# Kernel tuning notes

Measured on AMD Instinct MI355X. Metric: run time of the kernel, lower is better.

Reference implementation:

```python
import jax, jax.numpy as jnp
import numpy as np

N_SRC = 50000
N_DST = 50000
N_EDGES = 800000
D_IN = 256
NUM_HEADS = 8
OUT_DIM = 16
NEG_SLOPE = 0.2


def setup_inputs() -> dict:
    key = jax.random.key(0)
    ks = jax.random.split(key, 9)
    feat_src = jax.random.normal(ks[0], (N_SRC, D_IN), dtype=jnp.float32)
    feat_dst = jax.random.normal(ks[1], (N_DST, D_IN), dtype=jnp.float32)
    W_src = jax.random.normal(ks[2], (NUM_HEADS * OUT_DIM, D_IN), dtype=jnp.float32) * 0.05
    b_src = jax.random.normal(ks[3], (NUM_HEADS * OUT_DIM,), dtype=jnp.float32) * 0.05
    W_dst = jax.random.normal(ks[4], (NUM_HEADS * OUT_DIM, D_IN), dtype=jnp.float32) * 0.05
    b_dst = jax.random.normal(ks[5], (NUM_HEADS * OUT_DIM,), dtype=jnp.float32) * 0.05
    attn = jax.random.normal(ks[6], (NUM_HEADS, 2 * OUT_DIM), dtype=jnp.float32) * 0.1
    src_idx = jax.random.randint(ks[7], (N_EDGES,), 0, N_SRC, dtype=jnp.int32)
    dst_idx = jax.random.randint(ks[8], (N_EDGES,), 0, N_DST, dtype=jnp.int32)
    return {"feat_src": feat_src, "feat_dst": feat_dst, "W_src": W_src,
            "b_src": b_src, "W_dst": W_dst, "b_dst": b_dst, "attn": attn,
            "src_idx": src_idx, "dst_idx": dst_idx}


def reference(feat_src, feat_dst, W_src, b_src, W_dst, b_dst, attn, src_idx, dst_idx):
    # Node-type-specific linear transforms (feat_drop=0 at inference)
    hs = (feat_src @ W_src.T + b_src).reshape(N_SRC, NUM_HEADS, OUT_DIM)
    hd = (feat_dst @ W_dst.T + b_dst).reshape(N_DST, NUM_HEADS, OUT_DIM)
    # Per-node attention logits: el_i = <hs_i, a_l>, er_j = <hd_j, a_r>
    el = jnp.einsum('nkd,kd->nk', hs, attn[:, :OUT_DIM])  # (N_src, K)
    er = jnp.einsum('nkd,kd->nk', hd, attn[:, OUT_DIM:])  # (N_dst, K)
    # Edge scores: e_uv = LeakyReLU(el_u + er_v)
    e = el[src_idx] + er[dst_idx]                          # (E, K)
    e = jnp.where(e >= 0, e, NEG_SLOPE * e)
    # Edge softmax over incoming edges of each destination node
    m = jax.ops.segment_max(e, dst_idx, num_segments=N_DST)        # (N_dst, K)
    e_exp = jnp.exp(e - m[dst_idx])
    denom = jax.ops.segment_sum(e_exp, dst_idx, num_segments=N_DST)
    a = e_exp / denom[dst_idx]                             # (E, K)
    # Weighted neighbor aggregation: sum_u a_uv * hs_u
    msg = hs[src_idx] * a[:, :, None]                      # (E, K, d_out)
    out = jax.ops.segment_sum(msg, dst_idx, num_segments=N_DST)
    return out.reshape(N_DST, NUM_HEADS * OUT_DIM)
```

## Files before the change

### kernel.cpp

```cpp
#include <hip/hip_runtime.h>
#include <hip/hip_bf16.h>

#define N_SRCC 50000
#define N_DSTC 50000
#define N_EDG 800000
#define NBUK 500
#define DPB 100
#define BCAP 2048
#define EPB 3334
#define NPB 240
#define GEMB 391

typedef __attribute__((ext_vector_type(8))) short bf16x8;
typedef __attribute__((ext_vector_type(4))) float f32x4;
typedef __attribute__((ext_vector_type(8))) unsigned short us8;

__device__ inline short f2bf(float x) {
  __hip_bfloat16 b = __float2bfloat16(x);
  return *reinterpret_cast<short*>(&b);
}
__device__ inline float bf2f(unsigned hi16) {
  union { unsigned u; float f; } c; c.u = hi16 << 16; return c.f;
}

__global__ void fold_kernel(const float* __restrict__ Wsrc, const float* __restrict__ bsrc,
                            const float* __restrict__ Wdst, const float* __restrict__ bdst,
                            const float* __restrict__ attn,
                            float* __restrict__ U, float* __restrict__ Cc,
                            short* __restrict__ Wbf, short* __restrict__ Ubf,
                            int* __restrict__ bCur) {
  int t = blockIdx.x * blockDim.x + threadIdx.x;
  if (t < 4096) {
    int side = t >> 11;
    int r = (t >> 8) & 7;
    int c = t & 255;
    const float* W = side ? Wdst : Wsrc;
    float s = 0.f;
    #pragma unroll
    for (int d = 0; d < 16; d++)
      s += attn[r*32 + side*16 + d] * W[(r*16 + d)*256 + c];
    U[t] = s;
    if (side == 1) Ubf[r*256 + c] = f2bf(s);
    else           Ubf[2048 + t]  = 0;
    const float4* p = (const float4*)&Wsrc[t*8];
    float4 v0 = p[0], v1 = p[1];
    bf16x8 w;
    w[0]=f2bf(v0.x); w[1]=f2bf(v0.y); w[2]=f2bf(v0.z); w[3]=f2bf(v0.w);
    w[4]=f2bf(v1.x); w[5]=f2bf(v1.y); w[6]=f2bf(v1.z); w[7]=f2bf(v1.w);
    *(bf16x8*)&Wbf[t*8] = w;
  }
  if (t < 16) {
    int side = t >> 3, r = t & 7;
    const float* b = side ? bdst : bsrc;
    float s = 0.f;
    #pragma unroll
    for (int d = 0; d < 16; d++) s += attn[r*32 + side*16 + d] * b[r*16 + d];
    Cc[t] = s;
  }
  if (t < NBUK) bCur[t] = 0;
}

__global__ __launch_bounds__(256) void mega(
    const float* __restrict__ feat_src, const float* __restrict__ feat_dst,
    const short* __restrict__ Wbf, const short* __restrict__ Ubf,
    const float* __restrict__ bias, const float* __restrict__ attn,
    const float* __restrict__ Cc,
    const int* __restrict__ src, const int* __restrict__ dst,
    int* __restrict__ bCur, unsigned* __restrict__ bData,
    __hip_bfloat16* __restrict__ hsC, float* __restrict__ el,
    float* __restrict__ er) {
  __shared__ __align__(16) char smem[20480];
  int b = blockIdx.x;
  int t = threadIdx.x;

  if (b < NPB) {
    int* h   = (int*)smem;
    int* cur = (int*)(smem + 2048);
    for (int i = t; i < NBUK; i += 256) h[i] = 0;
    __syncthreads();
    int start = b * EPB;
    int end = min(start + EPB, N_EDG);
    for (int e = start + t; e < end; e += 256)
      atomicAdd(&h[dst[e] / DPB], 1);
    __syncthreads();
    for (int i = t; i < NBUK; i += 256) {
      int c = h[i];
      cur[i] = c ? atomicAdd(&bCur[i], c) : 0;
    }
    __syncthreads();
    for (int e = start + t; e < end; e += 256) {
      int d = dst[e], bk = d / DPB;
      int pos = atomicAdd(&cur[bk], 1);
      if (pos < BCAP)
        bData[(size_t)bk*BCAP + pos] = (unsigned)src[e] | ((unsigned)(d - bk*DPB) << 16);
    }
    return;
  }

  if (b < NPB + GEMB) {
    short (*As)[40] = (short(*)[40])smem;
    short (*Bs)[40] = (short(*)[40])(smem + 10240);
    int lane = t & 63, wid = t >> 6;
    int wr = wid >> 1, wc = wid & 1;
    int row0 = (b - NPB) * 128;
    int lr = lane & 15, lk = lane >> 4;
    int sr = t >> 1, skq = (t & 1) * 16;
    int gr = row0 + sr;
    f32x4 acc[4][4] = {};
    float4 pa0 = {}, pa1 = {}, pa2 = {}, pa3 = {};
    bf16x8 pb0, pb1;

    #define LOADA_HS(K0) { \
      if (gr < N_SRCC) { \
        const float4* p = (const float4*)&feat_src[(size_t)gr*256 + (K0) + skq]; \
        pa0 = p[0]; pa1 = p[1]; pa2 = p[2]; pa3 = p[3]; \
      } \
    }
    #define LOADB_HS(K0) { \
      pb0 = *(const bf16x8*)&Wbf[sr*256 + (K0) + skq]; \
      pb1 = *(const bf16x8*)&Wbf[sr*256 + (K0) + skq + 8]; \
    }

    LOADA_HS(0); LOADB_HS(0);
    for (int k0 = 0; k0 < 256; k0 += 32) {
      {
        bf16x8 t0, t1;
        t0[0]=f2bf(pa0.x); t0[1]=f2bf(pa0.y); t0[2]=f2bf(pa0.z); t0[3]=f2bf(pa0.w);
        t0[4]=f2bf(pa1.x); t0[5]=f2bf(pa1.y); t0[6]=f2bf(pa1.z); t0[7]=f2bf(pa1.w);
        t1[0]=f2bf(pa2.x); t1[1]=f2bf(pa2.y); t1[2]=f2bf(pa2.z); t1[3]=f2bf(pa2.w);
        t1[4]=f2bf(pa3.x); t1[5]=f2bf(pa3.y); t1[6]=f2bf(pa3.z); t1[7]=f2bf(pa3.w);
        *(bf16x8*)&As[sr][skq]     = t0;
        *(bf16x8*)&As[sr][skq + 8] = t1;
        *(bf16x8*)&Bs[sr][skq]     = pb0;
        *(bf16x8*)&Bs[sr][skq + 8] = pb1;
      }
      __syncthreads();
      if (k0 < 224) { LOADA_HS(k0 + 32); LOADB_HS(k0 + 32); }
      bf16x8 af[4], bfr[4];
      #pragma unroll
      for (int m = 0; m < 4; m++)
        af[m] = *(const bf16x8*)&As[wr*64 + m*16 + lr][lk*8];
      #pragma unroll
      for (int n = 0; n < 4; n++)
        bfr[n] = *(const bf16x8*)&Bs[wc*64 + n*16 + lr][lk*8];
      #pragma unroll
      for (int m = 0; m < 4; m++)
        #pragma unroll
        for (int n = 0; n < 4; n++)
          acc[m][n] = __builtin_amdgcn_mfma_f32_16x16x32_bf16(af[m], bfr[n], acc[m][n], 0, 0, 0);
      __syncthreads();
    }
    #undef LOADA_HS
    #undef LOADB_HS
    #pragma unroll
    for (int m = 0; m < 4; m++) {
      int r0 = row0 + wr*64 + m*16 + lk*4;
      #pragma unroll
      for (int n = 0; n < 4; n++) {
        int col = wc*64 + n*16 + lr;
        int h = wc*4 + n;
        float bv = bias[col];
        float al = attn[h*32 + lr];
        #pragma unroll
        for (int j = 0; j < 4; j++) {
          int gr2 = r0 + j;
          float hv = acc[m][n][j] + bv;
          if (gr2 < N_SRCC) hsC[(size_t)gr2*128 + col] = __float2bfloat16(hv);
          float p = hv * al;
          p += __shfl_xor(p, 1); p += __shfl_xor(p, 2);
          p += __shfl_xor(p, 4); p += __shfl_xor(p, 8);
          if (lr == 0 && gr2 < N_SRCC) el[gr2*8 + h] = p;
        }
      }
    }
    return;
  }

  {
    short (*As)[40]  = (short(*)[40])smem;
    short (*Bu)[264] = (short(*)[264])(smem + 10240);
    int lane = t & 63, wid = t >> 6;
    int row0 = (b - NPB - GEMB) * 128;
    int lr = lane & 15, lk = lane >> 4;
    int sr = t >> 1, skq = (t & 1) * 16;
    int gr = row0 + sr;
    #pragma unroll
    for (int i = 0; i < 2; i++) {
      int c = t + i*256;
      int r = c >> 5, ck = c & 31;
      *(bf16x8*)&Bu[r][ck*8] = *(const bf16x8*)&Ubf[r*256 + ck*8];
    }
    f32x4 acc[2] = {};
    float4 pa0 = {}, pa1 = {}, pa2 = {}, pa3 = {};

    #define LOADA_ER(K0) { \
      if (gr < N_DSTC) { \
        const float4* p = (const float4*)&feat_dst[(size_t)gr*256 + (K0) + skq]; \
        pa0 = p[0]; pa1 = p[1]; pa2 = p[2]; pa3 = p[3]; \
      } \
    }

    LOADA_ER(0);
    for (int k0 = 0; k0 < 256; k0 += 32) {
      {
        bf16x8 t0, t1;
        t0[0]=f2bf(pa0.x); t0[1]=f2bf(pa0.y); t0[2]=f2bf(pa0.z); t0[3]=f2bf(pa0.w);
        t0[4]=f2bf(pa1.x); t0[5]=f2bf(pa1.y); t0[6]=f2bf(pa1.z); t0[7]=f2bf(pa1.w);
        t1[0]=f2bf(pa2.x); t1[1]=f2bf(pa2.y); t1[2]=f2bf(pa2.z); t1[3]=f2bf(pa2.w);
        t1[4]=f2bf(pa3.x); t1[5]=f2bf(pa3.y); t1[6]=f2bf(pa3.z); t1[7]=f2bf(pa3.w);
        *(bf16x8*)&As[sr][skq]     = t0;
        *(bf16x8*)&As[sr][skq + 8] = t1;
      }
      __syncthreads();
      if (k0 < 224) LOADA_ER(k0 + 32);
      bf16x8 bu = *(const bf16x8*)&Bu[lr][k0 + lk*8];
      #pragma unroll
      for (int m = 0; m < 2; m++) {
        bf16x8 af = *(const bf16x8*)&As[wid*32 + m*16 + lr][lk*8];
        acc[m] = __builtin_amdgcn_mfma_f32_16x16x32_bf16(af, bu, acc[m], 0, 0, 0);
      }
      __syncthreads();
    }
    #undef LOADA_ER
    if (lr < 8) {
      float cb = Cc[8 + lr];
      #pragma unroll
      for (int m = 0; m < 2; m++) {
        int r0 = row0 + wid*32 + m*16 + lk*4;
        #pragma unroll
        for (int j = 0; j < 4; j++) {
          int gr2 = r0 + j;
          if (gr2 < N_DSTC) er[gr2*8 + lr] = acc[m][j] + cb;
        }
      }
    }
  }
}

__global__ __launch_bounds__(256) void sort_bucket(const unsigned* __restrict__ bData,
    const int* __restrict__ bCur, int* __restrict__ offS, int* __restrict__ offE,
    unsigned short* __restrict__ srcS) {
  __shared__ int hist[DPB];
  __shared__ int s[128];
  __shared__ int cur[DPB];
  int b = blockIdx.x, t = threadIdx.x;
  int cnt = min(bCur[b], BCAP);
  int base = b * BCAP;
  for (int i = t; i < DPB; i += 256) hist[i] = 0;
  __syncthreads();
  for (int e = t; e < cnt; e += 256) atomicAdd(&hist[bData[base + e] >> 16], 1);
  __syncthreads();
  if (t < 128) s[t] = (t < DPB) ? hist[t] : 0;
  __syncthreads();
  for (int d = 1; d < 128; d <<= 1) {
    int v = (t < 128 && t >= d) ? s[t - d] : 0;
    __syncthreads();
    if (t < 128) s[t] += v;
    __syncthreads();
  }
  if (t < DPB) {
    int excl = s[t] - hist[t];
    cur[t] = excl;
    offS[b * DPB + t] = base + excl;
    offE[b * DPB + t] = base + excl + hist[t];
  }
  __syncthreads();
  for (int e = t; e < cnt; e += 256) {
    unsigned ent = bData[base + e];
    int pos = atomicAdd(&cur[ent >> 16], 1);
    srcS[base + pos] = (unsigned short)(ent & 0xffffu);
  }
}

__global__ __launch_bounds__(256) void aggregate(
    const __hip_bfloat16* __restrict__ hs, const float* __restrict__ el,
    const float* __restrict__ er, const int* __restrict__ offS,
    const int* __restrict__ offE, const unsigned short* __restrict__ srcS,
    float* __restrict__ out) {
  int w = threadIdx.x >> 6;
  int lane = threadIdx.x & 63;
  int jA = blockIdx.x * 8 + w;
  int jB = jA + 4;
  int g = lane >> 4;
  int q = lane & 15;
  int h = q >> 1;
  int e0a = offS[jA], remA = offE[jA] - e0a;
  int e0b = offS[jB], remB = offE[jB] - e0b;
  float erA = er[jA*8 + h];
  float erB = er[jB*8 + h];
  float accA[8] = {}, accB[8] = {};
  float denA = 0.f, denB = 0.f;

  #define AGG_BODY(E, ERH, ACC, DEN) { \
    int s = srcS[E]; \
    float ev = el[s*8 + h] + ERH; \
    ev = ev >= 0.f ? ev : 0.2f * ev; \
    float wg = __expf(ev); \
    DEN += wg; \
    us8 hv = *(const us8*)&hs[(size_t)s*128 + q*8]; \
    _Pragma("unroll") \
    for (int c = 0; c < 8; c++) { \
      ACC[c] = fmaf(wg, bf2f((unsigned)hv[c]), ACC[c]); \
    } \
  }

  int ka = 0, kb = 0;
  while (ka + 8 <= remA && kb + 8 <= remB) {
    AGG_BODY(e0a + ka + g, erA, accA, denA);
    AGG_BODY(e0b + kb + g, erB, accB, denB);
    AGG_BODY(e0a + ka + 4 + g, erA, accA, denA);
    AGG_BODY(e0b + kb + 4 + g, erB, accB, denB);
    ka += 8; kb += 8;
  }
  while (ka + 4 <= remA && kb + 4 <= remB) {
    AGG_BODY(e0a + ka + g, erA, accA, denA);
    AGG_BODY(e0b + kb + g, erB, accB, denB);
    ka += 4; kb += 4;
  }
  while (ka + 4 <= remA) { AGG_BODY(e0a + ka + g, erA, accA, denA); ka += 4; }
  while (kb + 4 <= remB) { AGG_BODY(e0b + kb + g, erB, accB, denB); kb += 4; }
  if (ka + g < remA) AGG_BODY(e0a + ka + g, erA, accA, denA);
  if (kb + g < remB) AGG_BODY(e0b + kb + g, erB, accB, denB);
  #undef AGG_BODY

  #pragma unroll
  for (int c = 0; c < 8; c++) {
    accA[c] += __shfl_xor(accA[c], 16); accA[c] += __shfl_xor(accA[c], 32);
    accB[c] += __shfl_xor(accB[c], 16); accB[c] += __shfl_xor(accB[c], 32);
  }
  denA += __shfl_xor(denA, 16); denA += __shfl_xor(denA, 32);
  denB += __shfl_xor(denB, 16); denB += __shfl_xor(denB, 32);
  if (g == 0) {
    float invA = (remA > 0) ? 1.f / denA : 0.f;
    float invB = (remB > 0) ? 1.f / denB : 0.f;
    float4 r0, r1;
    r0.x = accA[0]*invA; r0.y = accA[1]*invA; r0.z = accA[2]*invA; r0.w = accA[3]*invA;
    r1.x = accA[4]*invA; r1.y = accA[5]*invA; r1.z = accA[6]*invA; r1.w = accA[7]*invA;
    *(float4*)&out[(size_t)jA*128 + q*8]     = r0;
    *(float4*)&out[(size_t)jA*128 + q*8 + 4] = r1;
    r0.x = accB[0]*invB; r0.y = accB[1]*invB; r0.z = accB[2]*invB; r0.w = accB[3]*invB;
    r1.x = accB[4]*invB; r1.y = accB[5]*invB; r1.z = accB[6]*invB; r1.w = accB[7]*invB;
    *(float4*)&out[(size_t)jB*128 + q*8]     = r0;
    *(float4*)&out[(size_t)jB*128 + q*8 + 4] = r1;
  }
}

extern "C" void kernel_launch(void* const* d_in, const int* in_sizes, int n_in,
                              void* d_out, int out_size, void* d_ws, size_t ws_size,
                              hipStream_t stream) {
  const float* feat_src = (const float*)d_in[0];
  const float* feat_dst = (const float*)d_in[1];
  const float* W_src = (const float*)d_in[2];
  const float* b_src = (const float*)d_in[3];
  const float* W_dst = (const float*)d_in[4];
  const float* b_dst = (const float*)d_in[5];
  const float* attn  = (const float*)d_in[6];
  const int* src_idx = (const int*)d_in[7];
  const int* dst_idx = (const int*)d_in[8];
  float* out = (float*)d_out;

  __hip_bfloat16* hs_bf = (__hip_bfloat16*)d_ws;
  float* el = (float*)(hs_bf + (size_t)N_SRCC*128);
  float* er = el + (size_t)N_SRCC*8;
  float* U  = er + (size_t)N_DSTC*8;
  float* Cc = U + 4096;
  short* Wbf = (short*)(Cc + 16);
  short* Ubf = Wbf + 32768;
  int* bCur  = (int*)(Ubf + 4096);
  int* offS  = bCur + NBUK;
  int* offE  = offS + N_DSTC;
  unsigned* bData = (unsigned*)(offE + N_DSTC);
  unsigned short* srcS = (unsigned short*)(bData + (size_t)NBUK*BCAP);

  fold_kernel<<<16, 256, 0, stream>>>(W_src, b_src, W_dst, b_dst, attn, U, Cc, Wbf, Ubf, bCur);
  mega<<<NPB + 2*GEMB, 256, 0, stream>>>(feat_src, feat_dst, Wbf, Ubf, b_src, attn,
                                         Cc, src_idx, dst_idx, bCur, bData,
                                         hs_bf, el, er);
  sort_bucket<<<NBUK, 256, 0, stream>>>(bData, bCur, offS, offE, srcS);
  aggregate<<<(N_DSTC + 7)/8, 256, 0, stream>>>(hs_bf, el, er, offS, offE, srcS, out);
}
```

Before: 86.18 us.

## Fuse bucket sort and aggregation into one kernel using shared-memory sorted sources

Merges the per-bucket counting sort and the attention aggregation into a single kernel. Sorted source indices and per-destination offsets stay in shared memory instead of being written to and re-read from global memory. This removes a kernel launch and a global round trip. In exchange the grid drops to 500 blocks of 512 threads, each looping over its 100 destinations, which reduces parallelism for hiding gather latency.

```diff
diff --git a/kernel.cpp b/kernel.cpp
--- a/kernel.cpp
+++ b/kernel.cpp
@@ -237,111 +237,110 @@
   }
 }
 
-__global__ __launch_bounds__(256) void sort_bucket(const unsigned* __restrict__ bData,
-    const int* __restrict__ bCur, int* __restrict__ offS, int* __restrict__ offE,
-    unsigned short* __restrict__ srcS) {
+__global__ __launch_bounds__(512) void sortagg(
+    const unsigned* __restrict__ bData, const int* __restrict__ bCur,
+    const __hip_bfloat16* __restrict__ hs, const float* __restrict__ el,
+    const float* __restrict__ er, float* __restrict__ out) {
   __shared__ int hist[DPB];
-  __shared__ int s[128];
-  __shared__ int cur[DPB];
+  __shared__ int scan[128];
+  __shared__ int offs[DPB + 1];
+  __shared__ unsigned short srcL[BCAP];
   int b = blockIdx.x, t = threadIdx.x;
   int cnt = min(bCur[b], BCAP);
   int base = b * BCAP;
-  for (int i = t; i < DPB; i += 256) hist[i] = 0;
-  __syncthreads();
-  for (int e = t; e < cnt; e += 256) atomicAdd(&hist[bData[base + e] >> 16], 1);
-  __syncthreads();
-  if (t < 128) s[t] = (t < DPB) ? hist[t] : 0;
+
+  for (int i = t; i < DPB; i += 512) hist[i] = 0;
+  __syncthreads();
+  for (int e = t; e < cnt; e += 512) atomicAdd(&hist[bData[base + e] >> 16], 1);
+  __syncthreads();
+  if (t < 128) scan[t] = (t < DPB) ? hist[t] : 0;
   __syncthreads();
   for (int d = 1; d < 128; d <<= 1) {
-    int v = (t < 128 && t >= d) ? s[t - d] : 0;
-    __syncthreads();
-    if (t < 128) s[t] += v;
-    __syncthreads();
-  }
-  if (t < DPB) {
-    int excl = s[t] - hist[t];
-    cur[t] = excl;
-    offS[b * DPB + t] = base + excl;
-    offE[b * DPB + t] = base + excl + hist[t];
-  }
-  __syncthreads();
-  for (int e = t; e < cnt; e += 256) {
+    int v = (t < 128 && t >= d) ? scan[t - d] : 0;
+    __syncthreads();
+    if (t < 128) scan[t] += v;
+    __syncthreads();
+  }
+  if (t < DPB) offs[t] = scan[t] - hist[t];
+  if (t == 0) offs[DPB] = cnt;
+  __syncthreads();
+  if (t < DPB) hist[t] = offs[t];
+  __syncthreads();
+  for (int e = t; e < cnt; e += 512) {
     unsigned ent = bData[base + e];
-    int pos = atomicAdd(&cur[ent >> 16], 1);
-    srcS[base + pos] = (unsigned short)(ent & 0xffffu);
-  }
-}
-
-__global__ __launch_bounds__(256) void aggregate(
-    const __hip_bfloat16* __restrict__ hs, const float* __restrict__ el,
-    const float* __restrict__ er, const int* __restrict__ offS,
-    const int* __restrict__ offE, const unsigned short* __restrict__ srcS,
-    float* __restrict__ out) {
-  int w = threadIdx.x >> 6;
-  int lane = threadIdx.x & 63;
-  int jA = blockIdx.x * 8 + w;
-  int jB = jA + 4;
+    int pos = atomicAdd(&hist[ent >> 16], 1);
+    srcL[pos] = (unsigned short)(ent & 0xffffu);
+  }
+  __syncthreads();
+
+  int w = t >> 6, lane = t & 63;
   int g = lane >> 4;
   int q = lane & 15;
   int h = q >> 1;
-  int e0a = offS[jA], remA = offE[jA] - e0a;
-  int e0b = offS[jB], remB = offE[jB] - e0b;
-  float erA = er[jA*8 + h];
-  float erB = er[jB*8 + h];
-  float accA[8] = {}, accB[8] = {};
-  float denA = 0.f, denB = 0.f;
-
-  #define AGG_BODY(E, ERH, ACC, DEN) { \
-    int s = srcS[E]; \
-    float ev = el[s*8 + h] + ERH; \
-    ev = ev >= 0.f ? ev : 0.2f * ev; \
-    float wg = __expf(ev); \
-    DEN += wg; \
-    us8 hv = *(const us8*)&hs[(size_t)s*128 + q*8]; \
-    _Pragma("unroll") \
-    for (int c = 0; c < 8; c++) { \
-      ACC[c] = fmaf(wg, bf2f((unsigned)hv[c]), ACC[c]); \
-    } \
-  }
-
-  int ka = 0, kb = 0;
-  while (ka + 8 <= remA && kb + 8 <= remB) {
-    AGG_BODY(e0a + ka + g, erA, accA, denA);
-    AGG_BODY(e0b + kb + g, erB, accB, denB);
-    AGG_BODY(e0a + ka + 4 + g, erA, accA, denA);
-    AGG_BODY(e0b + kb + 4 + g, erB, accB, denB);
-    ka += 8; kb += 8;
-  }
-  while (ka + 4 <= remA && kb + 4 <= remB) {
-    AGG_BODY(e0a + ka + g, erA, accA, denA);
-    AGG_BODY(e0b + kb + g, erB, accB, denB);
-    ka += 4; kb += 4;
-  }
-  while (ka + 4 <= remA) { AGG_BODY(e0a + ka + g, erA, accA, denA); ka += 4; }
-  while (kb + 4 <= remB) { AGG_BODY(e0b + kb + g, erB, accB, denB); kb += 4; }
-  if (ka + g < remA) AGG_BODY(e0a + ka + g, erA, accA, denA);
-  if (kb + g < remB) AGG_BODY(e0b + kb + g, erB, accB, denB);
-  #undef AGG_BODY
-
-  #pragma unroll
-  for (int c = 0; c < 8; c++) {
-    accA[c] += __shfl_xor(accA[c], 16); accA[c] += __shfl_xor(accA[c], 32);
-    accB[c] += __shfl_xor(accB[c], 16); accB[c] += __shfl_xor(accB[c], 32);
-  }
-  denA += __shfl_xor(denA, 16); denA += __shfl_xor(denA, 32);
-  denB += __shfl_xor(denB, 16); denB += __shfl_xor(denB, 32);
-  if (g == 0) {
-    float invA = (remA > 0) ? 1.f / denA : 0.f;
-    float invB = (remB > 0) ? 1.f / denB : 0.f;
-    float4 r0, r1;
-    r0.x = accA[0]*invA; r0.y = accA[1]*invA; r0.z = accA[2]*invA; r0.w = accA[3]*invA;
-    r1.x = accA[4]*invA; r1.y = accA[5]*invA; r1.z = accA[6]*invA; r1.w = accA[7]*invA;
-    *(float4*)&out[(size_t)jA*128 + q*8]     = r0;
-    *(float4*)&out[(size_t)jA*128 + q*8 + 4] = r1;
-    r0.x = accB[0]*invB; r0.y = accB[1]*invB; r0.z = accB[2]*invB; r0.w = accB[3]*invB;
-    r1.x = accB[4]*invB; r1.y = accB[5]*invB; r1.z = accB[6]*invB; r1.w = accB[7]*invB;
-    *(float4*)&out[(size_t)jB*128 + q*8]     = r0;
-    *(float4*)&out[(size_t)jB*128 + q*8 + 4] = r1;
+  int d0 = b * DPB;
+
+  for (int p = w; p < 50; p += 8) {
+    int dA = p, dB = p + 50;
+    int jA = d0 + dA, jB = d0 + dB;
+    int e0a = offs[dA], remA = offs[dA + 1] - e0a;
+    int e0b = offs[dB], remB = offs[dB + 1] - e0b;
+    float erA = er[jA*8 + h];
+    float erB = er[jB*8 + h];
+    float accA[8] = {}, accB[8] = {};
+    float denA = 0.f, denB = 0.f;
+
+    #define AGG_BODY(E, ERH, ACC, DEN) { \
+      int s = srcL[E]; \
+      float ev = el[s*8 + h] + ERH; \
+      ev = ev >= 0.f ? ev : 0.2f * ev; \
+      float wg = __expf(ev); \
+      DEN += wg; \
+      us8 hv = *(const us8*)&hs[(size_t)s*128 + q*8]; \
+      _Pragma("unroll") \
+      for (int c = 0; c < 8; c++) { \
+        ACC[c] = fmaf(wg, bf2f((unsigned)hv[c]), ACC[c]); \
+      } \
+    }
+
+    int ka = 0, kb = 0;
+    while (ka + 8 <= remA && kb + 8 <= remB) {
+      AGG_BODY(e0a + ka + g, erA, accA, denA);
+      AGG_BODY(e0b + kb + g, erB, accB, denB);
+      AGG_BODY(e0a + ka + 4 + g, erA, accA, denA);
+      AGG_BODY(e0b + kb + 4 + g, erB, accB, denB);
+      ka += 8; kb += 8;
+    }
+    while (ka + 4 <= remA && kb + 4 <= remB) {
+      AGG_BODY(e0a + ka + g, erA, accA, denA);
+      AGG_BODY(e0b + kb + g, erB, accB, denB);
+      ka += 4; kb += 4;
+    }
+    while (ka + 4 <= remA) { AGG_BODY(e0a + ka + g, erA, accA, denA); ka += 4; }
+    while (kb + 4 <= remB) { AGG_BODY(e0b + kb + g, erB, accB, denB); kb += 4; }
+    if (ka + g < remA) AGG_BODY(e0a + ka + g, erA, accA, denA);
+    if (kb + g < remB) AGG_BODY(e0b + kb + g, erB, accB, denB);
+    #undef AGG_BODY
+
+    #pragma unroll
+    for (int c = 0; c < 8; c++) {
+      accA[c] += __shfl_xor(accA[c], 16); accA[c] += __shfl_xor(accA[c], 32);
+      accB[c] += __shfl_xor(accB[c], 16); accB[c] += __shfl_xor(accB[c], 32);
+    }
+    denA += __shfl_xor(denA, 16); denA += __shfl_xor(denA, 32);
+    denB += __shfl_xor(denB, 16); denB += __shfl_xor(denB, 32);
+    if (g == 0) {
+      float invA = (remA > 0) ? 1.f / denA : 0.f;
+      float invB = (remB > 0) ? 1.f / denB : 0.f;
+      float4 r0, r1;
+      r0.x = accA[0]*invA; r0.y = accA[1]*invA; r0.z = accA[2]*invA; r0.w = accA[3]*invA;
+      r1.x = accA[4]*invA; r1.y = accA[5]*invA; r1.z = accA[6]*invA; r1.w = accA[7]*invA;
+      *(float4*)&out[(size_t)jA*128 + q*8]     = r0;
+      *(float4*)&out[(size_t)jA*128 + q*8 + 4] = r1;
+      r0.x = accB[0]*invB; r0.y = accB[1]*invB; r0.z = accB[2]*invB; r0.w = accB[3]*invB;
+      r1.x = accB[4]*invB; r1.y = accB[5]*invB; r1.z = accB[6]*invB; r1.w = accB[7]*invB;
+      *(float4*)&out[(size_t)jB*128 + q*8]     = r0;
+      *(float4*)&out[(size_t)jB*128 + q*8 + 4] = r1;
+    }
   }
 }
 
@@ -367,15 +366,12 @@
   short* Wbf = (short*)(Cc + 16);
   short* Ubf = Wbf + 32768;
   int* bCur  = (int*)(Ubf + 4096);
-  int* offS  = bCur + NBUK;
-  int* offE  = offS + N_DSTC;
-  unsigned* bData = (unsigned*)(offE + N_DSTC);
-  unsigned short* srcS = (unsigned short*)(bData + (size_t)NBUK*BCAP);
-
-  fold_kernel<<<16, 256, 0, stream>>>(W_src, b_src, W_dst, b_dst, attn, U, Cc, Wbf, Ubf, bCur);
+  unsigned* bData = (unsigned*)(bCur + NBUK);
+
+  fold_kernel<<<16, 256, 0, stream>>>(W_src, b_src, W_dst, b_dst, attn, U, Cc,
+                                      Wbf, Ubf, bCur);
   mega<<<NPB + 2*GEMB, 256, 0, stream>>>(feat_src, feat_dst, Wbf, Ubf, b_src, attn,
                                          Cc, src_idx, dst_idx, bCur, bData,
                                          hs_bf, el, er);
-  sort_bucket<<<NBUK, 256, 0, stream>>>(bData, bCur, offS, offE, srcS);
-  aggregate<<<(N_DSTC + 7)/8, 256, 0, stream>>>(hs_bf, el, er, offS, offE, srcS, out);
-}
+  sortagg<<<NBUK, 512, 0, stream>>>(bData, bCur, hs_bf, el, er, out);
+}
```

New measurement: 81.18 us, median of 2. 5.8% less time.
